# Kernel optimization log

Hardware: AMD Instinct MI355X
Metric: run time of the kernel (lower is better)

Reference implementation:

```python
import jax, jax.numpy as jnp
import numpy as np

DIM = 256      # dim_hidden * 2
HEADS = 8      # hier_tf_head
C = 256        # out_channels per head (concat=False)
FF = 1024      # dim_hidden * 8
N_HOPS = 4096
HOP_LEN = 12
N_MEM = N_HOPS * HOP_LEN
N = N_HOPS + N_MEM  # 53248 total nodes


def setup_inputs() -> dict:
    key = jax.random.key(0)
    ks = jax.random.split(key, 8)
    x = jax.random.normal(ks[0], (N, DIM), jnp.float32)
    # hop_attn structure built by the python loops: [j,j] self-edges for hop
    # tokens, then one edge (member_node -> hop_token) per member.
    hop_self = np.stack([np.arange(N_HOPS), np.arange(N_HOPS)])
    mem_src = np.arange(N_HOPS, N)
    mem_dst = np.arange(N_MEM) // HOP_LEN
    edge_index = jnp.asarray(
        np.concatenate([hop_self, np.stack([mem_src, mem_dst])], axis=1),
        jnp.int32)  # [2, E]

    def init(k, shp, fan):
        return jax.random.normal(k, shp, jnp.float32) / np.sqrt(fan).astype(np.float32)

    return {
        "x": x,
        "edge_index": edge_index,
        "gat_W": init(ks[1], (DIM, HEADS * C), DIM),
        "gat_att_src": init(ks[2], (HEADS, C), C),
        "gat_att_dst": init(ks[3], (HEADS, C), C),
        "gat_bias": jnp.zeros((C,), jnp.float32),
        "ffn_W1": init(ks[4], (DIM, FF), DIM),
        "ffn_b1": jnp.zeros((FF,), jnp.float32),
        "ffn_W2": init(ks[5], (FF, DIM), FF),
        "ffn_b2": jnp.zeros((DIM,), jnp.float32),
        "ln1_g": jnp.ones((DIM,), jnp.float32),
        "ln1_b": jnp.zeros((DIM,), jnp.float32),
        "ln2_g": jnp.ones((DIM,), jnp.float32),
        "ln2_b": jnp.zeros((DIM,), jnp.float32),
    }


def _layer_norm(x, g, b, eps=1e-5):
    mu = jnp.mean(x, axis=-1, keepdims=True)
    var = jnp.mean(jnp.square(x - mu), axis=-1, keepdims=True)
    return (x - mu) * jax.lax.rsqrt(var + eps) * g + b


def _gat_conv(x, src, dst, W, att_src, att_dst, bias):
    # PyG GATConv, concat=False (mean over heads), negative_slope=0.2
    h = (x @ W).reshape(N, HEADS, C)                       # [N,H,C]
    a_s = jnp.einsum('nhc,hc->nh', h, att_src)             # [N,H]
    a_d = jnp.einsum('nhc,hc->nh', h, att_dst)
    e = jax.nn.leaky_relu(a_s[src] + a_d[dst], 0.2)        # [E,H]
    m = jax.ops.segment_max(e, dst, num_segments=N)        # per-dst softmax
    e = jnp.exp(e - m[dst])
    denom = jax.ops.segment_sum(e, dst, num_segments=N)
    alpha = e / (denom[dst] + 1e-16)                       # [E,H]
    agg = jax.ops.segment_sum(h[src] * alpha[:, :, None], dst, num_segments=N)
    return agg.mean(axis=1) + bias                         # [N,DIM]


def reference(x, edge_index, gat_W, gat_att_src, gat_att_dst, gat_bias,
              ffn_W1, ffn_b1, ffn_W2, ffn_b2, ln1_g, ln1_b, ln2_g, ln2_b):
    # GATConv adds self-loops for every node by default
    loops = jnp.arange(N, dtype=edge_index.dtype)
    src = jnp.concatenate([edge_index[0], loops])
    dst = jnp.concatenate([edge_index[1], loops])
    # GAT + residual + LN (dropout is identity at eval)
    g_out = _gat_conv(x, src, dst, gat_W, gat_att_src, gat_att_dst, gat_bias)
    x1 = _layer_norm(g_out + x, ln1_g, ln1_b)
    # FFN + residual + LN
    ff = jax.nn.relu(x1 @ ffn_W1 + ffn_b1) @ ffn_W2 + ffn_b2
    return _layer_norm(ff + x1, ln2_g, ln2_b)
```

## Files before the change

### kernel.cpp

```cpp
#include <hip/hip_runtime.h>
#include <cstdint>
#include <cstddef>

#define N_TOT   53248
#define N_HOPS  4096
#define HOP_LEN 12
#define NHEAD   8
#define FFD     1024
#define GLD     384

typedef __bf16 bf16x8 __attribute__((ext_vector_type(8)));
typedef float f32x4 __attribute__((ext_vector_type(4)));

__device__ __forceinline__ unsigned short f2bf(float f) {
    unsigned int u = __float_as_uint(f);
    u += 0x7FFFu + ((u >> 16) & 1u);
    return (unsigned short)(u >> 16);
}
__device__ __forceinline__ float bf2f(unsigned short b) {
    return __uint_as_float((unsigned int)b << 16);
}
__device__ __forceinline__ void gload16(const void* g, void* l) {
    __builtin_amdgcn_global_load_lds(
        (const __attribute__((address_space(1))) void*)g,
        (__attribute__((address_space(3))) void*)l, 16, 0, 0);
}

__global__ __launch_bounds__(256) void prep_w(
    const float* __restrict__ W, const float* __restrict__ att_s,
    const float* __restrict__ att_d, unsigned short* __restrict__ BcT)
{
    int d = blockIdx.x, c = threadIdx.x;
    int wave = c >> 6;
    __shared__ float ps4[4], pd4[4];
    float wm = 0.f;
    for (int h = 0; h < NHEAD; ++h) {
        float w = W[d * 2048 + h * 256 + c];
        wm += w;
        float ps = w * att_s[h * 256 + c];
        float pd = w * att_d[h * 256 + c];
        for (int o = 32; o > 0; o >>= 1) {
            ps += __shfl_xor(ps, o);
            pd += __shfl_xor(pd, o);
        }
        if ((c & 63) == 0) { ps4[wave] = ps; pd4[wave] = pd; }
        __syncthreads();
        if (c == 0) BcT[(256 + h) * 256 + d] = f2bf(ps4[0] + ps4[1] + ps4[2] + ps4[3]);
        if (c == 1) BcT[(264 + h) * 256 + d] = f2bf(pd4[0] + pd4[1] + pd4[2] + pd4[3]);
        __syncthreads();
    }
    BcT[c * 256 + d] = f2bf(wm * 0.125f);
}

__global__ __launch_bounds__(256) void tconv(
    const float* __restrict__ in, unsigned short* __restrict__ out,
    int IS, int OS, int in_zoff, int out_zoff)
{
    __shared__ float t[32][33];
    in  += (size_t)blockIdx.z * in_zoff;
    out += (size_t)blockIdx.z * out_zoff;
    int tx = threadIdx.x, ty = threadIdx.y;
    int c0 = blockIdx.x * 32, r0 = blockIdx.y * 32;
    #pragma unroll
    for (int k = 0; k < 4; ++k)
        t[ty + 8 * k][tx] = in[(size_t)(r0 + ty + 8 * k) * IS + c0 + tx];
    __syncthreads();
    #pragma unroll
    for (int k = 0; k < 4; ++k)
        out[(size_t)(c0 + ty + 8 * k) * OS + r0 + tx] = f2bf(t[tx][ty + 8 * k]);
}

__global__ __launch_bounds__(256) void cvt_bf16(
    const float* __restrict__ in, unsigned short* __restrict__ out, int n4)
{
    int i = blockIdx.x * 256 + threadIdx.x;
    if (i >= n4) return;
    float4 v = ((const float4*)in)[i];
    ushort4 o;
    o.x = f2bf(v.x); o.y = f2bf(v.y); o.z = f2bf(v.z); o.w = f2bf(v.w);
    ((ushort4*)out)[i] = o;
}

__global__ __launch_bounds__(256) void hop_z(
    const unsigned short* __restrict__ xb, const unsigned short* __restrict__ gb,
    unsigned short* __restrict__ z)
{
    int j = blockIdx.x, tid = threadIdx.x;
    __shared__ float xr[13][256];
    __shared__ float sm[NHEAD][13];
    __shared__ float walpha[NHEAD][13];
    __shared__ float mxs[NHEAD], invs[NHEAD];

    for (int i = tid; i < 13 * 32; i += 256) {
        int r = i >> 5, c8 = (i & 31) * 8;
        int src = (r == 0) ? j : (N_HOPS + j * HOP_LEN + r - 1);
        uint4 u = *(const uint4*)&xb[(size_t)src * 256 + c8];
        float4 lo, hi;
        lo.x = bf2f((unsigned short)(u.x & 0xFFFF)); lo.y = bf2f((unsigned short)(u.x >> 16));
        lo.z = bf2f((unsigned short)(u.y & 0xFFFF)); lo.w = bf2f((unsigned short)(u.y >> 16));
        hi.x = bf2f((unsigned short)(u.z & 0xFFFF)); hi.y = bf2f((unsigned short)(u.z >> 16));
        hi.z = bf2f((unsigned short)(u.w & 0xFFFF)); hi.w = bf2f((unsigned short)(u.w >> 16));
        *(float4*)&xr[r][c8] = lo;
        *(float4*)&xr[r][c8 + 4] = hi;
    }
    if (tid < NHEAD * 13) {
        int h = tid / 13, k = tid % 13;
        int src = (k == 0) ? j : (N_HOPS + j * HOP_LEN + k - 1);
        float ad = bf2f(gb[(size_t)j * GLD + 264 + h]);
        float v = bf2f(gb[(size_t)src * GLD + 256 + h]) + ad;
        sm[h][k] = v > 0.f ? v : 0.2f * v;
    }
    __syncthreads();
    if (tid < NHEAD) {
        int h = tid;
        float mx = sm[h][0];
        for (int k = 1; k < 13; ++k) mx = fmaxf(mx, sm[h][k]);
        float sum = 2.f * expf(sm[h][0] - mx);
        for (int k = 1; k < 13; ++k) sum += expf(sm[h][k] - mx);
        mxs[h] = mx;
        invs[h] = 0.125f / (sum + 1e-16f);
    }
    __syncthreads();
    if (tid < NHEAD * 13) {
        int h = tid / 13, k = tid % 13;
        walpha[h][k] = (k == 0 ? 2.f : 1.f) * expf(sm[h][k] - mxs[h]) * invs[h];
    }
    __syncthreads();
    for (int h = 0; h < NHEAD; ++h) {
        float acc = 0.f;
        #pragma unroll
        for (int r = 0; r < 13; ++r) acc += walpha[h][r] * xr[r][tid];
        z[((size_t)j * NHEAD + h) * 256 + tid] = f2bf(acc);
    }
}

template <int RELU, int OUT_BF16>
__global__ __launch_bounds__(256) void gemm_bt(
    const unsigned short* __restrict__ A, const unsigned short* __restrict__ BT,
    const float* __restrict__ bias, void* __restrict__ Cout,
    int M, int Nc, int K, int ldc)
{
    __shared__ __align__(16) unsigned short As[128 * 32];
    __shared__ __align__(16) unsigned short Bs[128 * 32];
    const int tid = threadIdx.x;
    const int l = tid & 63;
    const int bm = blockIdx.y * 128, bn = blockIdx.x * 128;
    const int wm = ((tid >> 6) >> 1) * 64, wn = ((tid >> 6) & 1) * 64;

    const int r0 = tid >> 2, ke0 = (tid & 3) * 8;
    const int r1 = (256 + tid) >> 2, ke1 = ((256 + tid) & 3) * 8;
    const unsigned short* ga0 = A + (size_t)(bm + r0) * K + ke0;
    const unsigned short* ga1 = A + (size_t)(bm + r1) * K + ke1;
    const unsigned short* gb0 = BT + (size_t)(bn + r0) * K + ke0;
    const unsigned short* gb1 = BT + (size_t)(bn + r1) * K + ke1;

    f32x4 acc[4][4];
    #pragma unroll
    for (int m = 0; m < 4; ++m)
        #pragma unroll
        for (int n = 0; n < 4; ++n)
            acc[m][n] = (f32x4){0.f, 0.f, 0.f, 0.f};

    const int lrow = l & 15, lk8 = (l >> 4) * 8;

    for (int k0 = 0; k0 < K; k0 += 32) {
        gload16(ga0 + k0, &As[(size_t)tid * 8]);
        gload16(ga1 + k0, &As[(size_t)(256 + tid) * 8]);
        gload16(gb0 + k0, &Bs[(size_t)tid * 8]);
        gload16(gb1 + k0, &Bs[(size_t)(256 + tid) * 8]);
        __syncthreads();
        bf16x8 af[4], bfr[4];
        #pragma unroll
        for (int m = 0; m < 4; ++m)
            af[m] = *(const bf16x8*)&As[(wm + m * 16 + lrow) * 32 + lk8];
        #pragma unroll
        for (int n = 0; n < 4; ++n)
            bfr[n] = *(const bf16x8*)&Bs[(wn + n * 16 + lrow) * 32 + lk8];
        #pragma unroll
        for (int m = 0; m < 4; ++m)
            #pragma unroll
            for (int n = 0; n < 4; ++n)
                acc[m][n] = __builtin_amdgcn_mfma_f32_16x16x32_bf16(
                    af[m], bfr[n], acc[m][n], 0, 0, 0);
        __syncthreads();
    }

    const int orow = (l >> 4) * 4, ocol = l & 15;
    #pragma unroll
    for (int m = 0; m < 4; ++m) {
        int gr = bm + wm + m * 16 + orow;
        #pragma unroll
        for (int n = 0; n < 4; ++n) {
            int gc = bn + wn + n * 16 + ocol;
            float bv = bias[gc];
            #pragma unroll
            for (int r = 0; r < 4; ++r) {
                float v = acc[m][n][r] + bv;
                if (RELU) v = fmaxf(v, 0.f);
                if (OUT_BF16)
                    ((unsigned short*)Cout)[(size_t)(gr + r) * ldc + gc] = f2bf(v);
                else
                    ((float*)Cout)[(size_t)(gr + r) * ldc + gc] = v;
            }
        }
    }
}

__global__ __launch_bounds__(256) void gemm_bt_sk(
    const unsigned short* __restrict__ A, const unsigned short* __restrict__ BT,
    unsigned short* __restrict__ Cpart, int M, int Nc, int Ksl, int ldA)
{
    __shared__ __align__(16) unsigned short As[128 * 32];
    __shared__ __align__(16) unsigned short Bs[128 * 32];
    const int tid = threadIdx.x;
    const int l = tid & 63;
    const int bm = blockIdx.y * 128, bn = blockIdx.x * 128;
    const int koff = blockIdx.z * Ksl;
    const int wm = ((tid >> 6) >> 1) * 64, wn = ((tid >> 6) & 1) * 64;

    const int r0 = tid >> 2, ke0 = (tid & 3) * 8;
    const int r1 = (256 + tid) >> 2, ke1 = ((256 + tid) & 3) * 8;
    const unsigned short* ga0 = A + (size_t)(bm + r0) * ldA + koff + ke0;
    const unsigned short* ga1 = A + (size_t)(bm + r1) * ldA + koff + ke1;
    const unsigned short* gb0 = BT + (size_t)(bn + r0) * ldA + koff + ke0;
    const unsigned short* gb1 = BT + (size_t)(bn + r1) * ldA + koff + ke1;

    f32x4 acc[4][4];
    #pragma unroll
    for (int m = 0; m < 4; ++m)
        #pragma unroll
        for (int n = 0; n < 4; ++n)
            acc[m][n] = (f32x4){0.f, 0.f, 0.f, 0.f};

    const int lrow = l & 15, lk8 = (l >> 4) * 8;

    for (int k0 = 0; k0 < Ksl; k0 += 32) {
        gload16(ga0 + k0, &As[(size_t)tid * 8]);
        gload16(ga1 + k0, &As[(size_t)(256 + tid) * 8]);
        gload16(gb0 + k0, &Bs[(size_t)tid * 8]);
        gload16(gb1 + k0, &Bs[(size_t)(256 + tid) * 8]);
        __syncthreads();
        bf16x8 af[4], bfr[4];
        #pragma unroll
        for (int m = 0; m < 4; ++m)
            af[m] = *(const bf16x8*)&As[(wm + m * 16 + lrow) * 32 + lk8];
        #pragma unroll
        for (int n = 0; n < 4; ++n)
            bfr[n] = *(const bf16x8*)&Bs[(wn + n * 16 + lrow) * 32 + lk8];
        #pragma unroll
        for (int m = 0; m < 4; ++m)
            #pragma unroll
            for (int n = 0; n < 4; ++n)
                acc[m][n] = __builtin_amdgcn_mfma_f32_16x16x32_bf16(
                    af[m], bfr[n], acc[m][n], 0, 0, 0);
        __syncthreads();
    }

    unsigned short* Cp = Cpart + (size_t)blockIdx.z * M * Nc;
    const int orow = (l >> 4) * 4, ocol = l & 15;
    #pragma unroll
    for (int m = 0; m < 4; ++m) {
        int gr = bm + wm + m * 16 + orow;
        #pragma unroll
        for (int n = 0; n < 4; ++n) {
            int gc = bn + wn + n * 16 + ocol;
            #pragma unroll
            for (int r = 0; r < 4; ++r)
                Cp[(size_t)(gr + r) * Nc + gc] = f2bf(acc[m][n][r]);
        }
    }
}

__global__ __launch_bounds__(256) void red_hop(
    const unsigned short* __restrict__ P, const float* __restrict__ bias,
    unsigned short* __restrict__ gbuf)
{
    int i = blockIdx.x * 256 + threadIdx.x;
    int row = i >> 6, c4 = (i & 63) * 4;
    float4 s = { 0.f, 0.f, 0.f, 0.f };
    #pragma unroll
    for (int zz = 0; zz < 8; ++zz) {
        ushort4 u = *(const ushort4*)&P[(size_t)zz * N_HOPS * 256 + (size_t)row * 256 + c4];
        s.x += bf2f(u.x); s.y += bf2f(u.y); s.z += bf2f(u.z); s.w += bf2f(u.w);
    }
    float4 bv = *(const float4*)&bias[c4];
    ushort4 o;
    o.x = f2bf(s.x + bv.x); o.y = f2bf(s.y + bv.y);
    o.z = f2bf(s.z + bv.z); o.w = f2bf(s.w + bv.w);
    *(ushort4*)&gbuf[(size_t)row * GLD + c4] = o;
}

__global__ __launch_bounds__(256) void ln_add_bb(
    const unsigned short* __restrict__ a, const unsigned short* __restrict__ b,
    const float* __restrict__ g, const float* __restrict__ be,
    unsigned short* __restrict__ outp)
{
    int wave = threadIdx.x >> 6, lane = threadIdx.x & 63;
    int n = blockIdx.x * 4 + wave;
    ushort4 av = *(const ushort4*)&a[(size_t)n * GLD + lane * 4];
    ushort4 bv = ((const ushort4*)b)[(size_t)n * 64 + lane];
    float v[4];
    v[0] = bf2f(av.x) + bf2f(bv.x); v[1] = bf2f(av.y) + bf2f(bv.y);
    v[2] = bf2f(av.z) + bf2f(bv.z); v[3] = bf2f(av.w) + bf2f(bv.w);
    float s = v[0] + v[1] + v[2] + v[3];
    for (int o = 32; o > 0; o >>= 1) s += __shfl_xor(s, o);
    float mu = s * (1.f / 256.f);
    float q = 0.f;
    #pragma unroll
    for (int i = 0; i < 4; ++i) { float d = v[i] - mu; q += d * d; }
    for (int o = 32; o > 0; o >>= 1) q += __shfl_xor(q, o);
    float rstd = rsqrtf(q * (1.f / 256.f) + 1e-5f);
    int c = lane * 4;
    float4 gv = *(const float4*)&g[c];
    float4 bev = *(const float4*)&be[c];
    ushort4 o4;
    o4.x = f2bf((v[0] - mu) * rstd * gv.x + bev.x);
    o4.y = f2bf((v[1] - mu) * rstd * gv.y + bev.y);
    o4.z = f2bf((v[2] - mu) * rstd * gv.z + bev.z);
    o4.w = f2bf((v[3] - mu) * rstd * gv.w + bev.w);
    ((ushort4*)outp)[(size_t)n * 64 + lane] = o4;
}

__global__ __launch_bounds__(512, 2) void fused_ffn(
    const unsigned short* __restrict__ x1b, const unsigned short* __restrict__ W1T,
    const float* __restrict__ b1, const unsigned short* __restrict__ W2T,
    const float* __restrict__ b2, const float* __restrict__ g2,
    const float* __restrict__ be2, float* __restrict__ out)
{
    __shared__ __align__(16) unsigned short sX1[8 * 128 * 32];
    __shared__ __align__(16) unsigned short sW1[8 * 64 * 32];
    __shared__ __align__(16) unsigned short sW2[2 * 256 * 32];
    __shared__ __align__(16) unsigned short sH[2 * 128 * 32];
    __shared__ float lnS[128][4], lnQ[128][4], lnMu[128], lnRs[128];

    const int tid = threadIdx.x, l = tid & 63, wid = tid >> 6;
    const int lrow = l & 15, hi16 = l >> 4;
    const int row0 = blockIdx.x * 128;
    const int wm1 = (wid >> 1) * 32, wn1 = (wid & 1) * 32;
    const int wm2 = (wid >> 2) * 64, wn2 = (wid & 3) * 64;

    float b2c[4], gc[4], bc[4];
    #pragma unroll
    for (int n = 0; n < 4; ++n) {
        int col = wn2 + n * 16 + lrow;
        b2c[n] = b2[col]; gc[n] = g2[col]; bc[n] = be2[col];
    }

    #pragma unroll
    for (int i = 0; i < 8; ++i) {
        int c = i * 512 + tid;
        int s = c >> 9, r = (c >> 2) & 127, q = c & 3;
        int gq = q ^ (r & 3);
        gload16(x1b + (size_t)(row0 + r) * 256 + s * 32 + gq * 8, &sX1[c * 8]);
    }
    #pragma unroll
    for (int i = 0; i < 4; ++i) {
        int c = i * 512 + tid;
        int s = c >> 8, hc = (c >> 2) & 63, q = c & 3;
        gload16(W1T + (size_t)hc * 256 + s * 32 + (q ^ (hc & 3)) * 8, &sW1[c * 8]);
    }
    #pragma unroll
    for (int i = 0; i < 4; ++i) {
        int c = i * 512 + tid;
        int k2 = c >> 10, fc = (c >> 2) & 255, q = c & 3;
        gload16(W2T + (size_t)fc * 1024 + k2 * 32 + (q ^ (fc & 3)) * 8, &sW2[c * 8]);
    }
    __syncthreads();

    f32x4 facc[4][4];
    #pragma unroll
    for (int m = 0; m < 4; ++m)
        #pragma unroll
        for (int n = 0; n < 4; ++n)
            facc[m][n] = (f32x4){0.f, 0.f, 0.f, 0.f};

    const int ra = wm1 + lrow, rb = wm1 + 16 + lrow;
    const int rc = wn1 + lrow, rd = wn1 + 16 + lrow;
    const int oa = ((hi16 ^ (ra & 3)) << 3), ob = ((hi16 ^ (rb & 3)) << 3);
    const int oc = ((hi16 ^ (rc & 3)) << 3), od = ((hi16 ^ (rd & 3)) << 3);

    for (int ch = 0; ch < 16; ++ch) {
        f32x4 hacc[2][2];
        #pragma unroll
        for (int m = 0; m < 2; ++m)
            #pragma unroll
            for (int n = 0; n < 2; ++n)
                hacc[m][n] = (f32x4){0.f, 0.f, 0.f, 0.f};
        #pragma unroll
        for (int ks = 0; ks < 8; ++ks) {
            bf16x8 a0 = *(const bf16x8*)&sX1[ks * 4096 + ra * 32 + oa];
            bf16x8 a1 = *(const bf16x8*)&sX1[ks * 4096 + rb * 32 + ob];
            bf16x8 w0 = *(const bf16x8*)&sW1[ks * 2048 + rc * 32 + oc];
            bf16x8 w1 = *(const bf16x8*)&sW1[ks * 2048 + rd * 32 + od];
            hacc[0][0] = __builtin_amdgcn_mfma_f32_16x16x32_bf16(a0, w0, hacc[0][0], 0, 0, 0);
            hacc[0][1] = __builtin_amdgcn_mfma_f32_16x16x32_bf16(a0, w1, hacc[0][1], 0, 0, 0);
            hacc[1][0] = __builtin_amdgcn_mfma_f32_16x16x32_bf16(a1, w0, hacc[1][0], 0, 0, 0);
            hacc[1][1] = __builtin_amdgcn_mfma_f32_16x16x32_bf16(a1, w1, hacc[1][1], 0, 0, 0);
        }
        #pragma unroll
        for (int n = 0; n < 2; ++n) {
            int hcol = wn1 + n * 16 + lrow;
            float bb = b1[ch * 64 + hcol];
            int k2 = hcol >> 5, kk = hcol & 31;
            #pragma unroll
            for (int m = 0; m < 2; ++m) {
                #pragma unroll
                for (int r = 0; r < 4; ++r) {
                    int row = wm1 + m * 16 + hi16 * 4 + r;
                    float v = fmaxf(hacc[m][n][r] + bb, 0.f);
                    sH[k2 * 4096 + row * 32 + ((((kk >> 3) ^ (row & 3)) << 3) | (kk & 7))] = f2bf(v);
                }
            }
        }
        __syncthreads();
        #pragma unroll
        for (int k2 = 0; k2 < 2; ++k2) {
            bf16x8 a[4];
            #pragma unroll
            for (int m = 0; m < 4; ++m) {
                int r = wm2 + m * 16 + lrow;
                a[m] = *(const bf16x8*)&sH[k2 * 4096 + r * 32 + ((hi16 ^ (r & 3)) << 3)];
            }
            #pragma unroll
            for (int n = 0; n < 4; ++n) {
                int r = wn2 + n * 16 + lrow;
                bf16x8 w = *(const bf16x8*)&sW2[k2 * 8192 + r * 32 + ((hi16 ^ (r & 3)) << 3)];
                #pragma unroll
                for (int m = 0; m < 4; ++m)
                    facc[m][n] = __builtin_amdgcn_mfma_f32_16x16x32_bf16(a[m], w, facc[m][n], 0, 0, 0);
            }
        }
        __syncthreads();
        if (ch < 15) {
            int c2 = ch + 1;
            #pragma unroll
            for (int i = 0; i < 4; ++i) {
                int c = i * 512 + tid;
                int s = c >> 8, hc = (c >> 2) & 63, q = c & 3;
                gload16(W1T + (size_t)(c2 * 64 + hc) * 256 + s * 32 + (q ^ (hc & 3)) * 8, &sW1[c * 8]);
            }
            #pragma unroll
            for (int i = 0; i < 4; ++i) {
                int c = i * 512 + tid;
                int k2 = c >> 10, fc = (c >> 2) & 255, q = c & 3;
                gload16(W2T + (size_t)fc * 1024 + c2 * 64 + k2 * 32 + (q ^ (fc & 3)) * 8, &sW2[c * 8]);
            }
            __syncthreads();
        }
    }

    #pragma unroll
    for (int m = 0; m < 4; ++m) {
        #pragma unroll
        for (int n = 0; n < 4; ++n) {
            int col = wn2 + n * 16 + lrow;
            int s = col >> 5, kk = col & 31;
            #pragma unroll
            for (int r = 0; r < 4; ++r) {
                int row = wm2 + m * 16 + hi16 * 4 + r;
                float res = bf2f(sX1[s * 4096 + row * 32 +
                                     ((((kk >> 3) ^ (row & 3)) << 3) | (kk & 7))]);
                facc[m][n][r] += b2c[n] + res;
            }
        }
    }
    #pragma unroll
    for (int m = 0; m < 4; ++m) {
        #pragma unroll
        for (int r = 0; r < 4; ++r) {
            float s = 0.f, q = 0.f;
            #pragma unroll
            for (int n = 0; n < 4; ++n) { float v = facc[m][n][r]; s += v; q += v * v; }
            #pragma unroll
            for (int o = 8; o >= 1; o >>= 1) { s += __shfl_xor(s, o); q += __shfl_xor(q, o); }
            if (lrow == 0) {
                int row = wm2 + m * 16 + hi16 * 4 + r;
                lnS[row][wid & 3] = s; lnQ[row][wid & 3] = q;
            }
        }
    }
    __syncthreads();
    if (tid < 128) {
        float s = lnS[tid][0] + lnS[tid][1] + lnS[tid][2] + lnS[tid][3];
        float q = lnQ[tid][0] + lnQ[tid][1] + lnQ[tid][2] + lnQ[tid][3];
        float mu = s * (1.f / 256.f);
        lnMu[tid] = mu;
        lnRs[tid] = rsqrtf(q * (1.f / 256.f) - mu * mu + 1e-5f);
    }
    __syncthreads();
    #pragma unroll
    for (int m = 0; m < 4; ++m) {
        #pragma unroll
        for (int r = 0; r < 4; ++r) {
            int row = wm2 + m * 16 + hi16 * 4 + r;
            float mu = lnMu[row], rs = lnRs[row];
            #pragma unroll
            for (int n = 0; n < 4; ++n) {
                int col = wn2 + n * 16 + lrow;
                out[(size_t)(row0 + row) * 256 + col] =
                    (facc[m][n][r] - mu) * rs * gc[n] + bc[n];
            }
        }
    }
}

extern "C" void kernel_launch(void* const* d_in, const int* in_sizes, int n_in,
                              void* d_out, int out_size, void* d_ws, size_t ws_size,
                              hipStream_t stream)
{
    const float* x       = (const float*)d_in[0];
    const float* gat_W   = (const float*)d_in[2];
    const float* att_src = (const float*)d_in[3];
    const float* att_dst = (const float*)d_in[4];
    const float* gat_b   = (const float*)d_in[5];
    const float* W1      = (const float*)d_in[6];
    const float* b1      = (const float*)d_in[7];
    const float* W2      = (const float*)d_in[8];
    const float* b2      = (const float*)d_in[9];
    const float* ln1_g   = (const float*)d_in[10];
    const float* ln1_b   = (const float*)d_in[11];
    const float* ln2_g   = (const float*)d_in[12];
    const float* ln2_b   = (const float*)d_in[13];
    float* out = (float*)d_out;

    char* p = (char*)d_ws;
    auto carve = [&p](size_t bytes) { char* r = p; p += (bytes + 255) & ~(size_t)255; return r; };
    unsigned short* gbuf = (unsigned short*)carve((size_t)N_TOT * GLD * 2);
    unsigned short* x1b  = (unsigned short*)carve((size_t)N_TOT * 256 * 2);
    unsigned short* z    = (unsigned short*)carve((size_t)N_HOPS * 2048 * 2);
    unsigned short* hopP = (unsigned short*)carve((size_t)8 * N_HOPS * 256 * 2);
    unsigned short* BcT  = (unsigned short*)carve((size_t)GLD * 256 * 2);
    unsigned short* B2T  = (unsigned short*)carve((size_t)2048 * 256 * 2);
    unsigned short* W1T  = (unsigned short*)carve((size_t)FFD * 256 * 2);
    unsigned short* W2T  = (unsigned short*)carve((size_t)256 * FFD * 2);
    float*          bias384 = (float*)carve(GLD * 4);

    hipMemsetAsync(BcT + 272 * 256, 0, (size_t)(GLD - 272) * 256 * 2, stream);
    hipMemcpyAsync(bias384, gat_b, 256 * 4, hipMemcpyDeviceToDevice, stream);
    hipMemsetAsync(bias384 + 256, 0, (GLD - 256) * 4, stream);
    hipLaunchKernelGGL(prep_w, dim3(256), dim3(256), 0, stream,
                       gat_W, att_src, att_dst, BcT);
    hipLaunchKernelGGL(tconv, dim3(8, 8, 8), dim3(32, 8), 0, stream,
                       gat_W, B2T, 2048, 2048, 256, 256);
    hipLaunchKernelGGL(tconv, dim3(32, 8, 1), dim3(32, 8), 0, stream,
                       W1, W1T, 1024, 256, 0, 0);
    hipLaunchKernelGGL(tconv, dim3(8, 32, 1), dim3(32, 8), 0, stream,
                       W2, W2T, 256, 1024, 0, 0);
    hipLaunchKernelGGL(cvt_bf16, dim3(N_TOT * 256 / 4 / 256), dim3(256), 0, stream,
                       x, x1b, N_TOT * 256 / 4);
    hipLaunchKernelGGL((gemm_bt<0, 1>), dim3(GLD / 128, N_TOT / 128), dim3(256), 0, stream,
                       x1b, BcT, bias384, gbuf, N_TOT, GLD, 256, GLD);
    hipLaunchKernelGGL(hop_z, dim3(N_HOPS), dim3(256), 0, stream,
                       x1b, gbuf, z);
    hipLaunchKernelGGL(gemm_bt_sk, dim3(2, N_HOPS / 128, 8), dim3(256), 0, stream,
                       z, B2T, hopP, N_HOPS, 256, 256, 2048);
    hipLaunchKernelGGL(red_hop, dim3(N_HOPS * 64 / 256), dim3(256), 0, stream,
                       hopP, gat_b, gbuf);
    hipLaunchKernelGGL(ln_add_bb, dim3(N_TOT / 4), dim3(256), 0, stream,
                       gbuf, x1b, ln1_g, ln1_b, x1b);
    hipLaunchKernelGGL(fused_ffn, dim3(N_TOT / 128), dim3(512), 0, stream,
                       x1b, W1T, b1, W2T, b2, ln2_g, ln2_b, out);
    (void)in_sizes; (void)n_in; (void)out_size; (void)ws_size;
}
```

Before: 232.9 us.

## Restructure fused FFN to 64-row tiles with 32x32 MFMA and register-held activations

The fused FFN kernel is rewritten to process 64 rows per 256-thread block instead of 128 rows per 512 threads. It uses 32x32x16 MFMA instructions, keeps the x1 activation rows in registers rather than LDS, and stages the whole 64-column W1 chunk and W2 chunk in LDS. The next W1 chunk load is issued before the second GEMM so it overlaps with that compute. The change aims to cut LDS traffic and instruction count per MFMA, but it doubles weight reloads per output row and raises register pressure from the 16-register activation array plus the 16-wide accumulators.

```diff
diff --git a/kernel.cpp b/kernel.cpp
--- a/kernel.cpp
+++ b/kernel.cpp
@@ -11,6 +11,7 @@
 
 typedef __bf16 bf16x8 __attribute__((ext_vector_type(8)));
 typedef float f32x4 __attribute__((ext_vector_type(4)));
+typedef float f32x16 __attribute__((ext_vector_type(16)));
 
 __device__ __forceinline__ unsigned short f2bf(float f) {
     unsigned int u = __float_as_uint(f);
@@ -321,187 +322,180 @@
     ((ushort4*)outp)[(size_t)n * 64 + lane] = o4;
 }
 
-__global__ __launch_bounds__(512, 2) void fused_ffn(
+__global__ __launch_bounds__(256, 2) void fused_ffn(
     const unsigned short* __restrict__ x1b, const unsigned short* __restrict__ W1T,
     const float* __restrict__ b1, const unsigned short* __restrict__ W2T,
     const float* __restrict__ b2, const float* __restrict__ g2,
     const float* __restrict__ be2, float* __restrict__ out)
 {
-    __shared__ __align__(16) unsigned short sX1[8 * 128 * 32];
-    __shared__ __align__(16) unsigned short sW1[8 * 64 * 32];
-    __shared__ __align__(16) unsigned short sW2[2 * 256 * 32];
-    __shared__ __align__(16) unsigned short sH[2 * 128 * 32];
-    __shared__ float lnS[128][4], lnQ[128][4], lnMu[128], lnRs[128];
-
-    const int tid = threadIdx.x, l = tid & 63, wid = tid >> 6;
-    const int lrow = l & 15, hi16 = l >> 4;
-    const int row0 = blockIdx.x * 128;
-    const int wm1 = (wid >> 1) * 32, wn1 = (wid & 1) * 32;
-    const int wm2 = (wid >> 2) * 64, wn2 = (wid & 3) * 64;
-
-    float b2c[4], gc[4], bc[4];
-    #pragma unroll
-    for (int n = 0; n < 4; ++n) {
-        int col = wn2 + n * 16 + lrow;
-        b2c[n] = b2[col]; gc[n] = g2[col]; bc[n] = be2[col];
-    }
+    __shared__ __align__(16) char smem[78848];
+    unsigned short* sW1u = (unsigned short*)smem;
+    unsigned short* sW2u = (unsigned short*)(smem + 32768);
+    unsigned short* sHu  = (unsigned short*)(smem + 65536);
+    float*          sB1  = (float*)(smem + 74752);
+
+    const int tid = threadIdx.x, l = tid & 63, w = tid >> 6;
+    const int l31 = l & 31, h1 = l >> 5;
+    const int row0 = blockIdx.x * 64;
+    const int rh  = w >> 1;
+    const int ch1 = (w & 1) * 32;
+    const int hc  = ch1 + l31;
 
     #pragma unroll
     for (int i = 0; i < 8; ++i) {
-        int c = i * 512 + tid;
-        int s = c >> 9, r = (c >> 2) & 127, q = c & 3;
-        int gq = q ^ (r & 3);
-        gload16(x1b + (size_t)(row0 + r) * 256 + s * 32 + gq * 8, &sX1[c * 8]);
-    }
-    #pragma unroll
-    for (int i = 0; i < 4; ++i) {
-        int c = i * 512 + tid;
-        int s = c >> 8, hc = (c >> 2) & 63, q = c & 3;
-        gload16(W1T + (size_t)hc * 256 + s * 32 + (q ^ (hc & 3)) * 8, &sW1[c * 8]);
-    }
-    #pragma unroll
-    for (int i = 0; i < 4; ++i) {
-        int c = i * 512 + tid;
-        int k2 = c >> 10, fc = (c >> 2) & 255, q = c & 3;
-        gload16(W2T + (size_t)fc * 1024 + k2 * 32 + (q ^ (fc & 3)) * 8, &sW2[c * 8]);
-    }
-    __syncthreads();
-
-    f32x4 facc[4][4];
-    #pragma unroll
-    for (int m = 0; m < 4; ++m)
-        #pragma unroll
-        for (int n = 0; n < 4; ++n)
-            facc[m][n] = (f32x4){0.f, 0.f, 0.f, 0.f};
-
-    const int ra = wm1 + lrow, rb = wm1 + 16 + lrow;
-    const int rc = wn1 + lrow, rd = wn1 + 16 + lrow;
-    const int oa = ((hi16 ^ (ra & 3)) << 3), ob = ((hi16 ^ (rb & 3)) << 3);
-    const int oc = ((hi16 ^ (rc & 3)) << 3), od = ((hi16 ^ (rd & 3)) << 3);
+        int c = i * 256 + tid;
+        int r = c >> 5, s = c & 31;
+        gload16(W1T + (size_t)r * 256 + ((s ^ (r & 7)) * 8), sW1u + c * 8);
+    }
+    #pragma unroll
+    for (int i = 0; i < 8; ++i) {
+        int c = i * 256 + tid;
+        int r = c >> 3, s = c & 7;
+        gload16(W2T + (size_t)r * 1024 + ((s ^ (r & 7)) * 8), sW2u + c * 8);
+    }
+    {
+        float4 bv = ((const float4*)b1)[tid];
+        *(float4*)&sB1[tid * 4] = bv;
+    }
+    bf16x8 a[16];
+    {
+        const unsigned short* xr = x1b + (size_t)(row0 + rh * 32 + l31) * 256 + h1 * 8;
+        #pragma unroll
+        for (int ks = 0; ks < 16; ++ks)
+            a[ks] = *(const bf16x8*)(xr + ks * 16);
+    }
+    f32x16 facc[2][2];
+    #pragma unroll
+    for (int m = 0; m < 2; ++m)
+        #pragma unroll
+        for (int n = 0; n < 2; ++n)
+            facc[m][n] = (f32x16)(0.f);
+    __syncthreads();
 
     for (int ch = 0; ch < 16; ++ch) {
-        f32x4 hacc[2][2];
-        #pragma unroll
-        for (int m = 0; m < 2; ++m)
-            #pragma unroll
-            for (int n = 0; n < 2; ++n)
-                hacc[m][n] = (f32x4){0.f, 0.f, 0.f, 0.f};
-        #pragma unroll
-        for (int ks = 0; ks < 8; ++ks) {
-            bf16x8 a0 = *(const bf16x8*)&sX1[ks * 4096 + ra * 32 + oa];
-            bf16x8 a1 = *(const bf16x8*)&sX1[ks * 4096 + rb * 32 + ob];
-            bf16x8 w0 = *(const bf16x8*)&sW1[ks * 2048 + rc * 32 + oc];
-            bf16x8 w1 = *(const bf16x8*)&sW1[ks * 2048 + rd * 32 + od];
-            hacc[0][0] = __builtin_amdgcn_mfma_f32_16x16x32_bf16(a0, w0, hacc[0][0], 0, 0, 0);
-            hacc[0][1] = __builtin_amdgcn_mfma_f32_16x16x32_bf16(a0, w1, hacc[0][1], 0, 0, 0);
-            hacc[1][0] = __builtin_amdgcn_mfma_f32_16x16x32_bf16(a1, w0, hacc[1][0], 0, 0, 0);
-            hacc[1][1] = __builtin_amdgcn_mfma_f32_16x16x32_bf16(a1, w1, hacc[1][1], 0, 0, 0);
-        }
-        #pragma unroll
-        for (int n = 0; n < 2; ++n) {
-            int hcol = wn1 + n * 16 + lrow;
-            float bb = b1[ch * 64 + hcol];
-            int k2 = hcol >> 5, kk = hcol & 31;
-            #pragma unroll
-            for (int m = 0; m < 2; ++m) {
+        f32x16 hA = (f32x16)(0.f), hB = (f32x16)(0.f);
+        #pragma unroll
+        for (int ks = 0; ks < 16; ks += 2) {
+            bf16x8 w0 = *(const bf16x8*)&sW1u[hc * 256 + (((2 * ks + h1) ^ (hc & 7)) * 8)];
+            bf16x8 w1 = *(const bf16x8*)&sW1u[hc * 256 + (((2 * ks + 2 + h1) ^ (hc & 7)) * 8)];
+            hA = __builtin_amdgcn_mfma_f32_32x32x16_bf16(a[ks], w0, hA, 0, 0, 0);
+            hB = __builtin_amdgcn_mfma_f32_32x32x16_bf16(a[ks + 1], w1, hB, 0, 0, 0);
+        }
+        float b1v = sB1[ch * 64 + hc];
+        #pragma unroll
+        for (int reg = 0; reg < 16; ++reg) {
+            int r2 = rh * 32 + (reg & 3) + 8 * (reg >> 2) + 4 * h1;
+            float v = fmaxf(hA[reg] + hB[reg] + b1v, 0.f);
+            sHu[r2 * 72 + hc] = f2bf(v);
+        }
+        __syncthreads();
+        if (ch < 15) {
+            #pragma unroll
+            for (int i = 0; i < 8; ++i) {
+                int c = i * 256 + tid;
+                int r = c >> 5, s = c & 31;
+                gload16(W1T + (size_t)((ch + 1) * 64 + r) * 256 + ((s ^ (r & 7)) * 8),
+                        sW1u + c * 8);
+            }
+        }
+        #pragma unroll
+        for (int ks = 0; ks < 4; ++ks) {
+            bf16x8 am[2], bn[2];
+            #pragma unroll
+            for (int m = 0; m < 2; ++m)
+                am[m] = *(const bf16x8*)&sHu[(m * 32 + l31) * 72 + (2 * ks + h1) * 8];
+            #pragma unroll
+            for (int n = 0; n < 2; ++n) {
+                int fc = w * 64 + n * 32 + l31;
+                bn[n] = *(const bf16x8*)&sW2u[fc * 64 + (((2 * ks + h1) ^ (fc & 7)) * 8)];
+            }
+            #pragma unroll
+            for (int m = 0; m < 2; ++m)
                 #pragma unroll
-                for (int r = 0; r < 4; ++r) {
-                    int row = wm1 + m * 16 + hi16 * 4 + r;
-                    float v = fmaxf(hacc[m][n][r] + bb, 0.f);
-                    sH[k2 * 4096 + row * 32 + ((((kk >> 3) ^ (row & 3)) << 3) | (kk & 7))] = f2bf(v);
-                }
-            }
-        }
-        __syncthreads();
-        #pragma unroll
-        for (int k2 = 0; k2 < 2; ++k2) {
-            bf16x8 a[4];
-            #pragma unroll
-            for (int m = 0; m < 4; ++m) {
-                int r = wm2 + m * 16 + lrow;
-                a[m] = *(const bf16x8*)&sH[k2 * 4096 + r * 32 + ((hi16 ^ (r & 3)) << 3)];
-            }
-            #pragma unroll
-            for (int n = 0; n < 4; ++n) {
-                int r = wn2 + n * 16 + lrow;
-                bf16x8 w = *(const bf16x8*)&sW2[k2 * 8192 + r * 32 + ((hi16 ^ (r & 3)) << 3)];
-                #pragma unroll
-                for (int m = 0; m < 4; ++m)
-                    facc[m][n] = __builtin_amdgcn_mfma_f32_16x16x32_bf16(a[m], w, facc[m][n], 0, 0, 0);
-            }
+                for (int n = 0; n < 2; ++n)
+                    facc[m][n] = __builtin_amdgcn_mfma_f32_32x32x16_bf16(
+                        am[m], bn[n], facc[m][n], 0, 0, 0);
         }
         __syncthreads();
         if (ch < 15) {
-            int c2 = ch + 1;
-            #pragma unroll
-            for (int i = 0; i < 4; ++i) {
-                int c = i * 512 + tid;
-                int s = c >> 8, hc = (c >> 2) & 63, q = c & 3;
-                gload16(W1T + (size_t)(c2 * 64 + hc) * 256 + s * 32 + (q ^ (hc & 3)) * 8, &sW1[c * 8]);
-            }
-            #pragma unroll
-            for (int i = 0; i < 4; ++i) {
-                int c = i * 512 + tid;
-                int k2 = c >> 10, fc = (c >> 2) & 255, q = c & 3;
-                gload16(W2T + (size_t)fc * 1024 + c2 * 64 + k2 * 32 + (q ^ (fc & 3)) * 8, &sW2[c * 8]);
-            }
-            __syncthreads();
-        }
-    }
-
-    #pragma unroll
-    for (int m = 0; m < 4; ++m) {
-        #pragma unroll
-        for (int n = 0; n < 4; ++n) {
-            int col = wn2 + n * 16 + lrow;
-            int s = col >> 5, kk = col & 31;
-            #pragma unroll
-            for (int r = 0; r < 4; ++r) {
-                int row = wm2 + m * 16 + hi16 * 4 + r;
-                float res = bf2f(sX1[s * 4096 + row * 32 +
-                                     ((((kk >> 3) ^ (row & 3)) << 3) | (kk & 7))]);
-                facc[m][n][r] += b2c[n] + res;
-            }
-        }
-    }
-    #pragma unroll
-    for (int m = 0; m < 4; ++m) {
-        #pragma unroll
-        for (int r = 0; r < 4; ++r) {
-            float s = 0.f, q = 0.f;
-            #pragma unroll
-            for (int n = 0; n < 4; ++n) { float v = facc[m][n][r]; s += v; q += v * v; }
-            #pragma unroll
-            for (int o = 8; o >= 1; o >>= 1) { s += __shfl_xor(s, o); q += __shfl_xor(q, o); }
-            if (lrow == 0) {
-                int row = wm2 + m * 16 + hi16 * 4 + r;
-                lnS[row][wid & 3] = s; lnQ[row][wid & 3] = q;
-            }
-        }
-    }
-    __syncthreads();
-    if (tid < 128) {
-        float s = lnS[tid][0] + lnS[tid][1] + lnS[tid][2] + lnS[tid][3];
-        float q = lnQ[tid][0] + lnQ[tid][1] + lnQ[tid][2] + lnQ[tid][3];
+            #pragma unroll
+            for (int i = 0; i < 8; ++i) {
+                int c = i * 256 + tid;
+                int r = c >> 3, s = c & 7;
+                gload16(W2T + (size_t)r * 1024 + (ch + 1) * 64 + ((s ^ (r & 7)) * 8),
+                        sW2u + c * 8);
+            }
+        }
+    }
+
+    float b2c[2], g2c[2], be2c[2];
+    #pragma unroll
+    for (int n = 0; n < 2; ++n) {
+        int fc = w * 64 + n * 32 + l31;
+        b2c[n] = b2[fc]; g2c[n] = g2[fc]; be2c[n] = be2[fc];
+    }
+    if ((w & 1) == 0) {
+        int r = rh * 32 + l31;
+        #pragma unroll
+        for (int ks = 0; ks < 16; ++ks)
+            *(bf16x8*)&sW1u[r * 256 + (((2 * ks + h1) ^ (r & 7)) * 8)] = a[ks];
+    }
+    __syncthreads();
+    #pragma unroll
+    for (int m = 0; m < 2; ++m)
+        #pragma unroll
+        for (int n = 0; n < 2; ++n)
+            #pragma unroll
+            for (int reg = 0; reg < 16; ++reg) {
+                int r2 = m * 32 + (reg & 3) + 8 * (reg >> 2) + 4 * h1;
+                int fc = w * 64 + n * 32 + l31;
+                float res = bf2f(sW1u[r2 * 256 + ((((fc >> 3) ^ (r2 & 7)) * 8) | (fc & 7))]);
+                facc[m][n][reg] += b2c[n] + res;
+            }
+    float* lnS = (float*)sW2u;
+    float* lnQ = lnS + 256;
+    float* lnM = lnQ + 256;
+    float* lnR = lnM + 64;
+    #pragma unroll
+    for (int m = 0; m < 2; ++m)
+        #pragma unroll
+        for (int reg = 0; reg < 16; ++reg) {
+            float s = facc[m][0][reg] + facc[m][1][reg];
+            float q = facc[m][0][reg] * facc[m][0][reg]
+                    + facc[m][1][reg] * facc[m][1][reg];
+            #pragma unroll
+            for (int o = 16; o >= 1; o >>= 1) {
+                s += __shfl_xor(s, o);
+                q += __shfl_xor(q, o);
+            }
+            if (l31 == 0) {
+                int r2 = m * 32 + (reg & 3) + 8 * (reg >> 2) + 4 * h1;
+                lnS[r2 * 4 + w] = s;
+                lnQ[r2 * 4 + w] = q;
+            }
+        }
+    __syncthreads();
+    if (tid < 64) {
+        float s = lnS[tid * 4] + lnS[tid * 4 + 1] + lnS[tid * 4 + 2] + lnS[tid * 4 + 3];
+        float q = lnQ[tid * 4] + lnQ[tid * 4 + 1] + lnQ[tid * 4 + 2] + lnQ[tid * 4 + 3];
         float mu = s * (1.f / 256.f);
-        lnMu[tid] = mu;
-        lnRs[tid] = rsqrtf(q * (1.f / 256.f) - mu * mu + 1e-5f);
-    }
-    __syncthreads();
-    #pragma unroll
-    for (int m = 0; m < 4; ++m) {
-        #pragma unroll
-        for (int r = 0; r < 4; ++r) {
-            int row = wm2 + m * 16 + hi16 * 4 + r;
-            float mu = lnMu[row], rs = lnRs[row];
-            #pragma unroll
-            for (int n = 0; n < 4; ++n) {
-                int col = wn2 + n * 16 + lrow;
-                out[(size_t)(row0 + row) * 256 + col] =
-                    (facc[m][n][r] - mu) * rs * gc[n] + bc[n];
-            }
-        }
-    }
+        lnM[tid] = mu;
+        lnR[tid] = rsqrtf(q * (1.f / 256.f) - mu * mu + 1e-5f);
+    }
+    __syncthreads();
+    #pragma unroll
+    for (int m = 0; m < 2; ++m)
+        #pragma unroll
+        for (int reg = 0; reg < 16; ++reg) {
+            int r2 = m * 32 + (reg & 3) + 8 * (reg >> 2) + 4 * h1;
+            float mu = lnM[r2], rs = lnR[r2];
+            #pragma unroll
+            for (int n = 0; n < 2; ++n) {
+                int fc = w * 64 + n * 32 + l31;
+                out[(size_t)(row0 + r2) * 256 + fc] =
+                    (facc[m][n][reg] - mu) * rs * g2c[n] + be2c[n];
+            }
+        }
 }
 
 extern "C" void kernel_launch(void* const* d_in, const int* in_sizes, int n_in,
@@ -558,7 +552,7 @@
                        hopP, gat_b, gbuf);
     hipLaunchKernelGGL(ln_add_bb, dim3(N_TOT / 4), dim3(256), 0, stream,
                        gbuf, x1b, ln1_g, ln1_b, x1b);
-    hipLaunchKernelGGL(fused_ffn, dim3(N_TOT / 128), dim3(512), 0, stream,
+    hipLaunchKernelGGL(fused_ffn, dim3(N_TOT / 64), dim3(256), 0, stream,
                        x1b, W1T, b1, W2T, b2, ln2_g, ln2_b, out);
     (void)in_sizes; (void)n_in; (void)out_size; (void)ws_size;
 }
```

Result: faster. 213.0 us (-8.5%).

## Split fused FFN into GEMM1 with hidden buffer and GEMM2+LN kernel, add block swizzle

Applied to the files above, without the earlier changes.

Replaces the single fused FFN kernel, which keeps the hidden activation in shared memory, with two kernels. The first is a standard tiled GEMM that writes the ReLU hidden layer (N x 1024 bf16) to global memory. The second is a GEMM over K=1024 fused with bias, residual and LayerNorm. It also adds an XCD-style blockIdx swizzle to gemm_bt and to the new kernel. This trades the fused kernel's serialized per-chunk structure and low occupancy for roughly 200MB of extra HBM round-trip traffic. The new GEMM2 loop is unpipelined, with a sync on every 32-wide K step.

```diff
diff --git a/kernel.cpp b/kernel.cpp
--- a/kernel.cpp
+++ b/kernel.cpp
@@ -134,7 +134,7 @@
     }
 }
 
-template <int RELU, int OUT_BF16>
+template <int RELU, int OUT_BF16, int SWZ>
 __global__ __launch_bounds__(256) void gemm_bt(
     const unsigned short* __restrict__ A, const unsigned short* __restrict__ BT,
     const float* __restrict__ bias, void* __restrict__ Cout,
@@ -144,7 +144,16 @@
     __shared__ __align__(16) unsigned short Bs[128 * 32];
     const int tid = threadIdx.x;
     const int l = tid & 63;
-    const int bm = blockIdx.y * 128, bn = blockIdx.x * 128;
+    int bm, bn;
+    if (SWZ) {
+        int lid = blockIdx.x + gridDim.x * blockIdx.y;
+        int per = (gridDim.x * gridDim.y) >> 3;
+        int wg = (lid & 7) * per + (lid >> 3);
+        bm = (wg / gridDim.x) * 128;
+        bn = (wg % gridDim.x) * 128;
+    } else {
+        bm = blockIdx.y * 128; bn = blockIdx.x * 128;
+    }
     const int wm = ((tid >> 6) >> 1) * 64, wn = ((tid >> 6) & 1) * 64;
 
     const int r0 = tid >> 2, ke0 = (tid & 3) * 8;
@@ -321,187 +330,115 @@
     ((ushort4*)outp)[(size_t)n * 64 + lane] = o4;
 }
 
-__global__ __launch_bounds__(512, 2) void fused_ffn(
-    const unsigned short* __restrict__ x1b, const unsigned short* __restrict__ W1T,
-    const float* __restrict__ b1, const unsigned short* __restrict__ W2T,
-    const float* __restrict__ b2, const float* __restrict__ g2,
-    const float* __restrict__ be2, float* __restrict__ out)
-{
-    __shared__ __align__(16) unsigned short sX1[8 * 128 * 32];
-    __shared__ __align__(16) unsigned short sW1[8 * 64 * 32];
-    __shared__ __align__(16) unsigned short sW2[2 * 256 * 32];
-    __shared__ __align__(16) unsigned short sH[2 * 128 * 32];
-    __shared__ float lnS[128][4], lnQ[128][4], lnMu[128], lnRs[128];
+__global__ __launch_bounds__(512) void ffn2_ln(
+    const unsigned short* __restrict__ hid, const unsigned short* __restrict__ W2T,
+    const float* __restrict__ b2, const unsigned short* __restrict__ x1b,
+    const float* __restrict__ g2, const float* __restrict__ be2,
+    float* __restrict__ out)
+{
+    __shared__ __align__(16) unsigned short As[128 * 32];
+    __shared__ __align__(16) unsigned short Bs[256 * 32];
+    __shared__ float lnS[128][4], lnQ[128][4], lnM[128], lnR[128];
 
     const int tid = threadIdx.x, l = tid & 63, wid = tid >> 6;
-    const int lrow = l & 15, hi16 = l >> 4;
-    const int row0 = blockIdx.x * 128;
-    const int wm1 = (wid >> 1) * 32, wn1 = (wid & 1) * 32;
-    const int wm2 = (wid >> 2) * 64, wn2 = (wid & 3) * 64;
-
-    float b2c[4], gc[4], bc[4];
+    const int wr = wid >> 2, wc = wid & 3;
+    const int lrow = l & 15, lk8 = (l >> 4) * 8;
+    const int lid = blockIdx.x;
+    const int row0 = ((lid & 7) * (416 / 8) + (lid >> 3)) * 128;
+
+    const unsigned short* ga  = hid + (size_t)(row0 + (tid >> 2)) * FFD + (tid & 3) * 8;
+    const unsigned short* gb0 = W2T + (size_t)(tid >> 2) * FFD + (tid & 3) * 8;
+    const unsigned short* gb1 = W2T + (size_t)((512 + tid) >> 2) * FFD + ((512 + tid) & 3) * 8;
+
+    f32x4 acc[4][4];
+    #pragma unroll
+    for (int m = 0; m < 4; ++m)
+        #pragma unroll
+        for (int n = 0; n < 4; ++n)
+            acc[m][n] = (f32x4){0.f, 0.f, 0.f, 0.f};
+
+    for (int k0 = 0; k0 < FFD; k0 += 32) {
+        gload16(ga + k0,  &As[(size_t)tid * 8]);
+        gload16(gb0 + k0, &Bs[(size_t)tid * 8]);
+        gload16(gb1 + k0, &Bs[(size_t)(512 + tid) * 8]);
+        __syncthreads();
+        bf16x8 af[4], bfr[4];
+        #pragma unroll
+        for (int m = 0; m < 4; ++m)
+            af[m] = *(const bf16x8*)&As[(wr * 64 + m * 16 + lrow) * 32 + lk8];
+        #pragma unroll
+        for (int n = 0; n < 4; ++n)
+            bfr[n] = *(const bf16x8*)&Bs[(wc * 64 + n * 16 + lrow) * 32 + lk8];
+        #pragma unroll
+        for (int m = 0; m < 4; ++m)
+            #pragma unroll
+            for (int n = 0; n < 4; ++n)
+                acc[m][n] = __builtin_amdgcn_mfma_f32_16x16x32_bf16(
+                    af[m], bfr[n], acc[m][n], 0, 0, 0);
+        __syncthreads();
+    }
+
+    const int orow = (l >> 4) * 4, ocol = l & 15;
+    float b2c[4], g2c[4], be2c[4];
     #pragma unroll
     for (int n = 0; n < 4; ++n) {
-        int col = wn2 + n * 16 + lrow;
-        b2c[n] = b2[col]; gc[n] = g2[col]; bc[n] = be2[col];
-    }
-
-    #pragma unroll
-    for (int i = 0; i < 8; ++i) {
-        int c = i * 512 + tid;
-        int s = c >> 9, r = (c >> 2) & 127, q = c & 3;
-        int gq = q ^ (r & 3);
-        gload16(x1b + (size_t)(row0 + r) * 256 + s * 32 + gq * 8, &sX1[c * 8]);
-    }
-    #pragma unroll
-    for (int i = 0; i < 4; ++i) {
-        int c = i * 512 + tid;
-        int s = c >> 8, hc = (c >> 2) & 63, q = c & 3;
-        gload16(W1T + (size_t)hc * 256 + s * 32 + (q ^ (hc & 3)) * 8, &sW1[c * 8]);
-    }
-    #pragma unroll
-    for (int i = 0; i < 4; ++i) {
-        int c = i * 512 + tid;
-        int k2 = c >> 10, fc = (c >> 2) & 255, q = c & 3;
-        gload16(W2T + (size_t)fc * 1024 + k2 * 32 + (q ^ (fc & 3)) * 8, &sW2[c * 8]);
-    }
-    __syncthreads();
-
-    f32x4 facc[4][4];
+        int col = wc * 64 + n * 16 + ocol;
+        b2c[n] = b2[col]; g2c[n] = g2[col]; be2c[n] = be2[col];
+    }
     #pragma unroll
     for (int m = 0; m < 4; ++m)
         #pragma unroll
-        for (int n = 0; n < 4; ++n)
-            facc[m][n] = (f32x4){0.f, 0.f, 0.f, 0.f};
-
-    const int ra = wm1 + lrow, rb = wm1 + 16 + lrow;
-    const int rc = wn1 + lrow, rd = wn1 + 16 + lrow;
-    const int oa = ((hi16 ^ (ra & 3)) << 3), ob = ((hi16 ^ (rb & 3)) << 3);
-    const int oc = ((hi16 ^ (rc & 3)) << 3), od = ((hi16 ^ (rd & 3)) << 3);
-
-    for (int ch = 0; ch < 16; ++ch) {
-        f32x4 hacc[2][2];
-        #pragma unroll
-        for (int m = 0; m < 2; ++m)
-            #pragma unroll
-            for (int n = 0; n < 2; ++n)
-                hacc[m][n] = (f32x4){0.f, 0.f, 0.f, 0.f};
-        #pragma unroll
-        for (int ks = 0; ks < 8; ++ks) {
-            bf16x8 a0 = *(const bf16x8*)&sX1[ks * 4096 + ra * 32 + oa];
-            bf16x8 a1 = *(const bf16x8*)&sX1[ks * 4096 + rb * 32 + ob];
-            bf16x8 w0 = *(const bf16x8*)&sW1[ks * 2048 + rc * 32 + oc];
-            bf16x8 w1 = *(const bf16x8*)&sW1[ks * 2048 + rd * 32 + od];
-            hacc[0][0] = __builtin_amdgcn_mfma_f32_16x16x32_bf16(a0, w0, hacc[0][0], 0, 0, 0);
-            hacc[0][1] = __builtin_amdgcn_mfma_f32_16x16x32_bf16(a0, w1, hacc[0][1], 0, 0, 0);
-            hacc[1][0] = __builtin_amdgcn_mfma_f32_16x16x32_bf16(a1, w0, hacc[1][0], 0, 0, 0);
-            hacc[1][1] = __builtin_amdgcn_mfma_f32_16x16x32_bf16(a1, w1, hacc[1][1], 0, 0, 0);
-        }
-        #pragma unroll
-        for (int n = 0; n < 2; ++n) {
-            int hcol = wn1 + n * 16 + lrow;
-            float bb = b1[ch * 64 + hcol];
-            int k2 = hcol >> 5, kk = hcol & 31;
-            #pragma unroll
-            for (int m = 0; m < 2; ++m) {
-                #pragma unroll
-                for (int r = 0; r < 4; ++r) {
-                    int row = wm1 + m * 16 + hi16 * 4 + r;
-                    float v = fmaxf(hacc[m][n][r] + bb, 0.f);
-                    sH[k2 * 4096 + row * 32 + ((((kk >> 3) ^ (row & 3)) << 3) | (kk & 7))] = f2bf(v);
-                }
+        for (int r = 0; r < 4; ++r) {
+            int row = wr * 64 + m * 16 + orow + r;
+            #pragma unroll
+            for (int n = 0; n < 4; ++n) {
+                int col = wc * 64 + n * 16 + ocol;
+                float res = bf2f(x1b[(size_t)(row0 + row) * 256 + col]);
+                acc[m][n][r] += b2c[n] + res;
             }
         }
-        __syncthreads();
-        #pragma unroll
-        for (int k2 = 0; k2 < 2; ++k2) {
-            bf16x8 a[4];
-            #pragma unroll
-            for (int m = 0; m < 4; ++m) {
-                int r = wm2 + m * 16 + lrow;
-                a[m] = *(const bf16x8*)&sH[k2 * 4096 + r * 32 + ((hi16 ^ (r & 3)) << 3)];
+    #pragma unroll
+    for (int m = 0; m < 4; ++m)
+        #pragma unroll
+        for (int r = 0; r < 4; ++r) {
+            float s = 0.f, q = 0.f;
+            #pragma unroll
+            for (int n = 0; n < 4; ++n) {
+                float v = acc[m][n][r];
+                s += v; q += v * v;
             }
             #pragma unroll
-            for (int n = 0; n < 4; ++n) {
-                int r = wn2 + n * 16 + lrow;
-                bf16x8 w = *(const bf16x8*)&sW2[k2 * 8192 + r * 32 + ((hi16 ^ (r & 3)) << 3)];
-                #pragma unroll
-                for (int m = 0; m < 4; ++m)
-                    facc[m][n] = __builtin_amdgcn_mfma_f32_16x16x32_bf16(a[m], w, facc[m][n], 0, 0, 0);
+            for (int o = 8; o >= 1; o >>= 1) {
+                s += __shfl_xor(s, o);
+                q += __shfl_xor(q, o);
+            }
+            if (ocol == 0) {
+                int row = wr * 64 + m * 16 + orow + r;
+                lnS[row][wc] = s; lnQ[row][wc] = q;
             }
         }
-        __syncthreads();
-        if (ch < 15) {
-            int c2 = ch + 1;
-            #pragma unroll
-            for (int i = 0; i < 4; ++i) {
-                int c = i * 512 + tid;
-                int s = c >> 8, hc = (c >> 2) & 63, q = c & 3;
-                gload16(W1T + (size_t)(c2 * 64 + hc) * 256 + s * 32 + (q ^ (hc & 3)) * 8, &sW1[c * 8]);
-            }
-            #pragma unroll
-            for (int i = 0; i < 4; ++i) {
-                int c = i * 512 + tid;
-                int k2 = c >> 10, fc = (c >> 2) & 255, q = c & 3;
-                gload16(W2T + (size_t)fc * 1024 + c2 * 64 + k2 * 32 + (q ^ (fc & 3)) * 8, &sW2[c * 8]);
-            }
-            __syncthreads();
-        }
-    }
-
-    #pragma unroll
-    for (int m = 0; m < 4; ++m) {
-        #pragma unroll
-        for (int n = 0; n < 4; ++n) {
-            int col = wn2 + n * 16 + lrow;
-            int s = col >> 5, kk = col & 31;
-            #pragma unroll
-            for (int r = 0; r < 4; ++r) {
-                int row = wm2 + m * 16 + hi16 * 4 + r;
-                float res = bf2f(sX1[s * 4096 + row * 32 +
-                                     ((((kk >> 3) ^ (row & 3)) << 3) | (kk & 7))]);
-                facc[m][n][r] += b2c[n] + res;
-            }
-        }
-    }
-    #pragma unroll
-    for (int m = 0; m < 4; ++m) {
-        #pragma unroll
-        for (int r = 0; r < 4; ++r) {
-            float s = 0.f, q = 0.f;
-            #pragma unroll
-            for (int n = 0; n < 4; ++n) { float v = facc[m][n][r]; s += v; q += v * v; }
-            #pragma unroll
-            for (int o = 8; o >= 1; o >>= 1) { s += __shfl_xor(s, o); q += __shfl_xor(q, o); }
-            if (lrow == 0) {
-                int row = wm2 + m * 16 + hi16 * 4 + r;
-                lnS[row][wid & 3] = s; lnQ[row][wid & 3] = q;
-            }
-        }
-    }
     __syncthreads();
     if (tid < 128) {
         float s = lnS[tid][0] + lnS[tid][1] + lnS[tid][2] + lnS[tid][3];
         float q = lnQ[tid][0] + lnQ[tid][1] + lnQ[tid][2] + lnQ[tid][3];
         float mu = s * (1.f / 256.f);
-        lnMu[tid] = mu;
-        lnRs[tid] = rsqrtf(q * (1.f / 256.f) - mu * mu + 1e-5f);
+        lnM[tid] = mu;
+        lnR[tid] = rsqrtf(q * (1.f / 256.f) - mu * mu + 1e-5f);
     }
     __syncthreads();
     #pragma unroll
-    for (int m = 0; m < 4; ++m) {
+    for (int m = 0; m < 4; ++m)
         #pragma unroll
         for (int r = 0; r < 4; ++r) {
-            int row = wm2 + m * 16 + hi16 * 4 + r;
-            float mu = lnMu[row], rs = lnRs[row];
+            int row = wr * 64 + m * 16 + orow + r;
+            float mu = lnM[row], rs = lnR[row];
             #pragma unroll
             for (int n = 0; n < 4; ++n) {
-                int col = wn2 + n * 16 + lrow;
+                int col = wc * 64 + n * 16 + ocol;
                 out[(size_t)(row0 + row) * 256 + col] =
-                    (facc[m][n][r] - mu) * rs * gc[n] + bc[n];
+                    (acc[m][n][r] - mu) * rs * g2c[n] + be2c[n];
             }
         }
-    }
 }
 
 extern "C" void kernel_launch(void* const* d_in, const int* in_sizes, int n_in,
@@ -529,6 +466,7 @@
     unsigned short* x1b  = (unsigned short*)carve((size_t)N_TOT * 256 * 2);
     unsigned short* z    = (unsigned short*)carve((size_t)N_HOPS * 2048 * 2);
     unsigned short* hopP = (unsigned short*)carve((size_t)8 * N_HOPS * 256 * 2);
+    unsigned short* hid  = (unsigned short*)carve((size_t)N_TOT * FFD * 2);
     unsigned short* BcT  = (unsigned short*)carve((size_t)GLD * 256 * 2);
     unsigned short* B2T  = (unsigned short*)carve((size_t)2048 * 256 * 2);
     unsigned short* W1T  = (unsigned short*)carve((size_t)FFD * 256 * 2);
@@ -548,7 +486,7 @@
                        W2, W2T, 256, 1024, 0, 0);
     hipLaunchKernelGGL(cvt_bf16, dim3(N_TOT * 256 / 4 / 256), dim3(256), 0, stream,
                        x, x1b, N_TOT * 256 / 4);
-    hipLaunchKernelGGL((gemm_bt<0, 1>), dim3(GLD / 128, N_TOT / 128), dim3(256), 0, stream,
+    hipLaunchKernelGGL((gemm_bt<0, 1, 1>), dim3(GLD / 128, N_TOT / 128), dim3(256), 0, stream,
                        x1b, BcT, bias384, gbuf, N_TOT, GLD, 256, GLD);
     hipLaunchKernelGGL(hop_z, dim3(N_HOPS), dim3(256), 0, stream,
                        x1b, gbuf, z);
@@ -558,7 +496,9 @@
                        hopP, gat_b, gbuf);
     hipLaunchKernelGGL(ln_add_bb, dim3(N_TOT / 4), dim3(256), 0, stream,
                        gbuf, x1b, ln1_g, ln1_b, x1b);
-    hipLaunchKernelGGL(fused_ffn, dim3(N_TOT / 128), dim3(512), 0, stream,
-                       x1b, W1T, b1, W2T, b2, ln2_g, ln2_b, out);
+    hipLaunchKernelGGL((gemm_bt<1, 1, 1>), dim3(FFD / 128, N_TOT / 128), dim3(256), 0, stream,
+                       x1b, W1T, b1, hid, N_TOT, FFD, 256, FFD);
+    hipLaunchKernelGGL(ffn2_ln, dim3(N_TOT / 128), dim3(512), 0, stream,
+                       hid, W2T, b2, x1b, ln2_g, ln2_b, out);
     (void)in_sizes; (void)n_in; (void)out_size; (void)ws_size;
 }
```

New measurement: 239.8 us. 3.0% more time.
